# Performance work log

Measured on AMD Instinct MI355X. Metric: run time of the kernel, lower is better.

## Reference

```python
import jax, jax.numpy as jnp
import numpy as np

B, S, D_MODEL, D_FF = 4, 2048, 1024, 4096


def setup_inputs() -> dict:
    key = jax.random.key(0)
    ks = jax.random.split(key, 8)
    return {
        "x": jax.random.normal(ks[0], (B, S, D_MODEL), dtype=jnp.float32),
        "W1": jax.random.normal(ks[1], (D_MODEL, D_FF), dtype=jnp.float32) * (1.0 / np.sqrt(D_MODEL)),
        "b1": jnp.zeros((D_FF,), dtype=jnp.float32),
        "quantum_phases": jax.random.normal(ks[2], (D_FF,), dtype=jnp.float32) * (2.0 * np.pi),
        "quantum_weights_real": jax.random.normal(ks[3], (D_FF,), dtype=jnp.float32) * 0.1,
        "quantum_weights_imag": jax.random.normal(ks[4], (D_FF,), dtype=jnp.float32) * 0.1,
        "W2": jax.random.normal(ks[5], (D_FF, D_MODEL), dtype=jnp.float32) * (1.0 / np.sqrt(D_FF)),
        "b2": jnp.zeros((D_MODEL,), dtype=jnp.float32),
    }


def _quantum_transform(hidden, theta, w_real, w_imag):
    # hidden: [B,S,d_ff]; theta/w_real/w_imag: [d_ff] broadcast over channels
    imag = w_imag * jnp.sin(theta + hidden * 0.1)
    quantum_phase = jnp.cos(theta) * w_real + jnp.sin(theta) * w_imag  # [d_ff]
    return hidden + quantum_phase * imag * 0.1


def reference(x, W1, b1, quantum_phases, quantum_weights_real, quantum_weights_imag, W2, b2):
    hidden = jnp.einsum("bsd,df->bsf", x, W1) + b1  # [B,S,d_ff]
    q = _quantum_transform(hidden, quantum_phases, quantum_weights_real, quantum_weights_imag)
    act = jax.nn.relu(q)  # dropout is identity in eval mode
    return jnp.einsum("bsf,fd->bsd", act, W2) + b2
```

## Files before the change

### kernel.cpp

```cpp
#include <hip/hip_runtime.h>

typedef __bf16 bf16x8 __attribute__((ext_vector_type(8)));
typedef short  s16x8  __attribute__((ext_vector_type(8)));
typedef float  f32x4  __attribute__((ext_vector_type(4)));

#define DEVINL __device__ __forceinline__

DEVINL unsigned short f2bf(float f) {
  unsigned int u = __builtin_bit_cast(unsigned int, f);
  u += 0x7fffu + ((u >> 16) & 1u);
  return (unsigned short)(u >> 16);
}

DEVINL void async16(const void* g, void* l) {
  __builtin_amdgcn_global_load_lds(
      (const __attribute__((address_space(1))) unsigned int*)g,
      (__attribute__((address_space(3))) unsigned int*)l, 16, 0, 0);
}


__global__ void cvt_f32_bf16(const float* __restrict__ in,
                             unsigned short* __restrict__ out, int n4) {
  int i = blockIdx.x * blockDim.x + threadIdx.x;
  int stride = gridDim.x * blockDim.x;
  for (; i < n4; i += stride) {
    float4 v = ((const float4*)in)[i];
    ushort4 o;
    o.x = f2bf(v.x); o.y = f2bf(v.y); o.z = f2bf(v.z); o.w = f2bf(v.w);
    ((ushort4*)out)[i] = o;
  }
}

__global__ void transpose_cvt(const float* __restrict__ in,
                              unsigned short* __restrict__ out, int R, int C) {
  __shared__ unsigned short tile[32][33];
  int bc = blockIdx.x * 32, br = blockIdx.y * 32;
  int tx = threadIdx.x & 31, ty = threadIdx.x >> 5;
#pragma unroll
  for (int i = 0; i < 32; i += 8)
    tile[ty + i][tx] = f2bf(in[(size_t)(br + ty + i) * C + (bc + tx)]);
  __syncthreads();
#pragma unroll
  for (int i = 0; i < 32; i += 8)
    out[(size_t)(bc + ty + i) * R + (br + tx)] = tile[tx][ty + i];
}

__global__ void qconst(const float* __restrict__ theta,
                       const float* __restrict__ wre,
                       const float* __restrict__ wim,
                       float* __restrict__ c1, int n) {
  int i = blockIdx.x * blockDim.x + threadIdx.x;
  if (i < n) {
    float t = theta[i];
    c1[i] = (cosf(t) * wre[i] + sinf(t) * wim[i]) * wim[i] * 0.1f;
  }
}


template <int BM, int NT, bool FUSED>
__global__ __launch_bounds__(512, 2) void gemm8(
    const unsigned short* __restrict__ A,
    const unsigned short* __restrict__ Bt,
    const float* __restrict__ bias,
    const float* __restrict__ theta,
    const float* __restrict__ c1,
    void* __restrict__ Cout,
    int N, int nTilesN) {
  constexpr int K      = NT * 64;
  constexpr int WROWS  = BM / 2;
  constexpr int M_REP  = WROWS / 16;
  constexpr int MH     = M_REP / 2;
  constexpr int ABYTES = BM * 128;
  constexpr int AH     = ABYTES / 2;
  constexpr int AL     = AH / 8192;
  constexpr int BUFSZ  = ABYTES + 32768;
  static_assert(AL == 2 || AL == 1, "geometry");

  __shared__ __align__(16) char lds[2 * BUFSZ];

  int nwg = gridDim.x;
  int wg = blockIdx.x;
  int sw = (wg & 7) * (nwg >> 3) + (wg >> 3);
  int rowBase = (sw / nTilesN) * BM;
  int colBase = (sw % nTilesN) * 256;

  const int t = threadIdx.x;
  const int lane = t & 63;
  const int wid = t >> 6;
  const int wr = wid >> 2, wc = wid & 3;
  const int lr = lane & 15;
  const int lg = lane >> 4;
  const int r7 = lane & 7;

  const int srow = t >> 3;
  const int scolB = ((t & 7) * 16) ^ ((srow & 7) << 4);
  const unsigned short* aSrcB = A  + (size_t)(rowBase + srow) * K + (scolB >> 1);
  const unsigned short* bSrcB = Bt + (size_t)(colBase + srow) * K + (scolB >> 1);

  const int aRd = (wr * WROWS + lr) * 128 + ((lg ^ r7) << 4);
  const int bRd = ABYTES + (wc * 64 + lr) * 128 + ((lg ^ r7) << 4);

  f32x4 acc[M_REP][4] = {};
  bf16x8 a[MH][2], b[4][2];

#define STAGE_AU(S, U, P) do {                                              \
    _Pragma("unroll") for (int j = 0; j < AL; ++j)                          \
      async16(aSrcB + ((size_t)((U) * WROWS + j * 64) * K + (size_t)(S) * 64),\
              &lds[(P) * BUFSZ + (U) * AH + j * 8192 + t * 16]);            \
  } while (0)
#define STAGE_BU(S, U, P) do {                                              \
    _Pragma("unroll") for (int j = 0; j < 2; ++j)                           \
      async16(bSrcB + ((size_t)((U) * 128 + j * 64) * K + (size_t)(S) * 64),\
              &lds[(P) * BUFSZ + ABYTES + (U) * 16384 + j * 8192 + t * 16]);\
  } while (0)

#define LOAD_A(MHh, P)                                                      \
  _Pragma("unroll") for (int mi = 0; mi < MH; ++mi)                         \
  _Pragma("unroll") for (int ks = 0; ks < 2; ++ks)                          \
    a[mi][ks] = __builtin_bit_cast(bf16x8, *(const s16x8*)&lds[             \
        (P) * BUFSZ + ((aRd + ((MHh) * MH + mi) * 2048) ^ (ks << 6))])
#define LOAD_B(NHh, P)                                                      \
  _Pragma("unroll") for (int nn = 0; nn < 2; ++nn)                          \
  _Pragma("unroll") for (int ks = 0; ks < 2; ++ks)                          \
    b[(NHh) * 2 + nn][ks] = __builtin_bit_cast(bf16x8, *(const s16x8*)&lds[ \
        (P) * BUFSZ + ((bRd + ((NHh) * 2 + nn) * 2048) ^ (ks << 6))])

#define QUAD(MHh, NHh)                                                      \
  __builtin_amdgcn_s_setprio(1);                                            \
  _Pragma("unroll") for (int mi = 0; mi < MH; ++mi)                         \
  _Pragma("unroll") for (int nn = 0; nn < 2; ++nn)                          \
  _Pragma("unroll") for (int ks = 0; ks < 2; ++ks)                          \
    acc[(MHh) * MH + mi][(NHh) * 2 + nn] =                                  \
        __builtin_amdgcn_mfma_f32_16x16x32_bf16(                            \
            a[mi][ks], b[(NHh) * 2 + nn][ks],                               \
            acc[(MHh) * MH + mi][(NHh) * 2 + nn], 0, 0, 0);                 \
  __builtin_amdgcn_s_setprio(0)

#define BAR() __builtin_amdgcn_s_barrier()
#define LG0() asm volatile("s_waitcnt lgkmcnt(0)" ::: "memory")

#define TILE(T, P) do {                                                     \
                                                      \
    LOAD_A(0, P); LOAD_B(0, P);                                             \
    if ((T) + 1 < NT) STAGE_AU((T) + 1, 0, (P) ^ 1);                        \
    if (MH == 4) asm volatile("s_waitcnt lgkmcnt(8)" ::: "memory");         \
    BAR(); LG0(); QUAD(0, 0); BAR();                                        \
                                                      \
    LOAD_B(1, P);                                                           \
    if ((T) + 1 < NT) STAGE_AU((T) + 1, 1, (P) ^ 1);                        \
    BAR(); LG0(); QUAD(0, 1); BAR();                                        \
                                                      \
    LOAD_A(1, P);                                                           \
    if ((T) + 2 < NT) STAGE_BU((T) + 2, 0, P);                              \
    BAR(); LG0(); QUAD(1, 1); BAR();                                        \
                                    \
    if ((T) + 2 < NT) STAGE_BU((T) + 2, 1, P);                              \
    BAR(); QUAD(1, 0);                                                      \
    if ((T) + 2 < NT) {                                                     \
      asm volatile("s_waitcnt vmcnt(4)" ::: "memory");                      \
    } else if ((T) + 1 < NT) {                                              \
      asm volatile("s_waitcnt vmcnt(0)" ::: "memory");                      \
    }                                                                       \
    BAR();                                                                  \
  } while (0)

  STAGE_AU(0, 0, 0); STAGE_AU(0, 1, 0);
  STAGE_BU(0, 0, 0); STAGE_BU(0, 1, 0);
  STAGE_BU(1, 0, 1); STAGE_BU(1, 1, 1);
  asm volatile("s_waitcnt vmcnt(4)" ::: "memory");
  BAR();

  for (int T = 0; T < NT; T += 2) {
    TILE(T, 0);
    TILE(T + 1, 1);
  }

#undef TILE
#undef QUAD
#undef LOAD_A
#undef LOAD_B
#undef STAGE_AU
#undef STAGE_BU
#undef BAR
#undef LG0

  const int orow0 = rowBase + wr * WROWS + (lane >> 4) * 4;
  const int ocol0 = colBase + wc * 64 + lr;
#pragma unroll
  for (int ni = 0; ni < 4; ++ni) {
    int n = ocol0 + ni * 16;
    float bv = bias[n];
    float th = 0.f, cc = 0.f;
    if constexpr (FUSED) { th = theta[n]; cc = c1[n]; }
#pragma unroll
    for (int mi = 0; mi < M_REP; ++mi) {
#pragma unroll
      for (int r = 0; r < 4; ++r) {
        size_t m = (size_t)(orow0 + mi * 16 + r);
        float h = acc[mi][ni][r] + bv;
        if constexpr (FUSED) {
          float q = h + cc * __sinf(th + 0.1f * h);
          ((unsigned short*)Cout)[m * N + n] = f2bf(fmaxf(q, 0.f));
        } else {
          ((float*)Cout)[m * N + n] = h;
        }
      }
    }
  }
}


extern "C" void kernel_launch(void* const* d_in, const int* in_sizes, int n_in,
                              void* d_out, int out_size, void* d_ws,
                              size_t ws_size, hipStream_t stream) {
  const float* x     = (const float*)d_in[0];
  const float* W1    = (const float*)d_in[1];
  const float* b1    = (const float*)d_in[2];
  const float* theta = (const float*)d_in[3];
  const float* qwr   = (const float*)d_in[4];
  const float* qwi   = (const float*)d_in[5];
  const float* W2    = (const float*)d_in[6];
  const float* b2    = (const float*)d_in[7];
  float* out = (float*)d_out;

  const int M = 4 * 2048;
  const int DM = 1024, DF = 4096;

  size_t need = ((size_t)96 << 20) + DF * sizeof(float);
  if (ws_size < need) return;

  char* ws = (char*)d_ws;
  unsigned short* xb   = (unsigned short*)ws;
  unsigned short* w1t  = (unsigned short*)(ws + ((size_t)16 << 20));
  unsigned short* w2t  = (unsigned short*)(ws + ((size_t)24 << 20));
  unsigned short* actb = (unsigned short*)(ws + ((size_t)32 << 20));
  float* c1 = (float*)(ws + ((size_t)96 << 20));

  cvt_f32_bf16<<<2048, 256, 0, stream>>>(x, xb, M * DM / 4);
  transpose_cvt<<<dim3(DF / 32, DM / 32), 256, 0, stream>>>(W1, w1t, DM, DF);
  transpose_cvt<<<dim3(DM / 32, DF / 32), 256, 0, stream>>>(W2, w2t, DF, DM);
  qconst<<<DF / 256, 256, 0, stream>>>(theta, qwr, qwi, c1, DF);

  gemm8<256, 16, true><<<512, 512, 0, stream>>>(
      xb, w1t, b1, theta, c1, (void*)actb, DF, DF / 256);
  gemm8<128, 64, false><<<256, 512, 0, stream>>>(
      actb, w2t, b2, nullptr, nullptr, (void*)out, DM, DM / 256);
}
```

Baseline: 166.1 us.

## Make fused GEMM1 persistent over two column tiles and stage epilogue stores through LDS

GEMM1 now launches half as many workgroups, each handling two adjacent 256-column output tiles in sequence. The prologue loads for the second tile are issued before the first tile's epilogue, so the epilogue overlaps with the next loads. The fused epilogue writes bf16 results into an extra 16KB LDS scratch region with a swizzle, then emits 16-byte coalesced global stores instead of scattered 2-byte stores. The extra LDS may reduce occupancy, and the grid drops to 256 workgroups, which lowers parallelism.

```diff
diff --git a/kernel.cpp b/kernel.cpp
--- a/kernel.cpp
+++ b/kernel.cpp
@@ -57,7 +57,7 @@
 }
 
 
-template <int BM, int NT, bool FUSED>
+template <int BM, int NT, int REPS, bool FUSED>
 __global__ __launch_bounds__(512, 2) void gemm8(
     const unsigned short* __restrict__ A,
     const unsigned short* __restrict__ Bt,
@@ -74,15 +74,16 @@
   constexpr int AH     = ABYTES / 2;
   constexpr int AL     = AH / 8192;
   constexpr int BUFSZ  = ABYTES + 32768;
+  constexpr int LDSSZ  = 2 * BUFSZ + (FUSED ? 16384 : 0);
   static_assert(AL == 2 || AL == 1, "geometry");
 
-  __shared__ __align__(16) char lds[2 * BUFSZ];
+  __shared__ __align__(16) char lds[LDSSZ];
 
   int nwg = gridDim.x;
   int wg = blockIdx.x;
   int sw = (wg & 7) * (nwg >> 3) + (wg >> 3);
   int rowBase = (sw / nTilesN) * BM;
-  int colBase = (sw % nTilesN) * 256;
+  int colBase = (sw % nTilesN) * (256 * REPS);
 
   const int t = threadIdx.x;
   const int lane = t & 63;
@@ -100,17 +101,14 @@
   const int aRd = (wr * WROWS + lr) * 128 + ((lg ^ r7) << 4);
   const int bRd = ABYTES + (wc * 64 + lr) * 128 + ((lg ^ r7) << 4);
 
-  f32x4 acc[M_REP][4] = {};
-  bf16x8 a[MH][2], b[4][2];
-
 #define STAGE_AU(S, U, P) do {                                              \
     _Pragma("unroll") for (int j = 0; j < AL; ++j)                          \
       async16(aSrcB + ((size_t)((U) * WROWS + j * 64) * K + (size_t)(S) * 64),\
               &lds[(P) * BUFSZ + (U) * AH + j * 8192 + t * 16]);            \
   } while (0)
-#define STAGE_BU(S, U, P) do {                                              \
+#define STAGE_BU(SRC, S, U, P) do {                                         \
     _Pragma("unroll") for (int j = 0; j < 2; ++j)                           \
-      async16(bSrcB + ((size_t)((U) * 128 + j * 64) * K + (size_t)(S) * 64),\
+      async16((SRC) + ((size_t)((U) * 128 + j * 64) * K + (size_t)(S) * 64),\
               &lds[(P) * BUFSZ + ABYTES + (U) * 16384 + j * 8192 + t * 16]);\
   } while (0)
 
@@ -140,21 +138,17 @@
 #define LG0() asm volatile("s_waitcnt lgkmcnt(0)" ::: "memory")
 
 #define TILE(T, P) do {                                                     \
-                                                      \
     LOAD_A(0, P); LOAD_B(0, P);                                             \
     if ((T) + 1 < NT) STAGE_AU((T) + 1, 0, (P) ^ 1);                        \
     if (MH == 4) asm volatile("s_waitcnt lgkmcnt(8)" ::: "memory");         \
     BAR(); LG0(); QUAD(0, 0); BAR();                                        \
-                                                      \
     LOAD_B(1, P);                                                           \
     if ((T) + 1 < NT) STAGE_AU((T) + 1, 1, (P) ^ 1);                        \
     BAR(); LG0(); QUAD(0, 1); BAR();                                        \
-                                                      \
     LOAD_A(1, P);                                                           \
-    if ((T) + 2 < NT) STAGE_BU((T) + 2, 0, P);                              \
+    if ((T) + 2 < NT) STAGE_BU(bSrcR, (T) + 2, 0, P);                       \
     BAR(); LG0(); QUAD(1, 1); BAR();                                        \
-                                    \
-    if ((T) + 2 < NT) STAGE_BU((T) + 2, 1, P);                              \
+    if ((T) + 2 < NT) STAGE_BU(bSrcR, (T) + 2, 1, P);                       \
     BAR(); QUAD(1, 0);                                                      \
     if ((T) + 2 < NT) {                                                     \
       asm volatile("s_waitcnt vmcnt(4)" ::: "memory");                      \
@@ -165,14 +159,87 @@
   } while (0)
 
   STAGE_AU(0, 0, 0); STAGE_AU(0, 1, 0);
-  STAGE_BU(0, 0, 0); STAGE_BU(0, 1, 0);
-  STAGE_BU(1, 0, 1); STAGE_BU(1, 1, 1);
+  STAGE_BU(bSrcB, 0, 0, 0); STAGE_BU(bSrcB, 0, 1, 0);
+  STAGE_BU(bSrcB, 1, 0, 1); STAGE_BU(bSrcB, 1, 1, 1);
   asm volatile("s_waitcnt vmcnt(4)" ::: "memory");
   BAR();
 
-  for (int T = 0; T < NT; T += 2) {
-    TILE(T, 0);
-    TILE(T + 1, 1);
+  for (int rep = 0; rep < REPS; ++rep) {
+    const unsigned short* bSrcR = bSrcB + (size_t)rep * 256 * K;
+    f32x4 acc[M_REP][4] = {};
+    bf16x8 a[MH][2], b[4][2];
+
+    for (int T = 0; T < NT; T += 2) {
+      TILE(T, 0);
+      TILE(T + 1, 1);
+    }
+
+    if (rep + 1 < REPS) {
+      const unsigned short* bSrcN = bSrcB + (size_t)(rep + 1) * 256 * K;
+      STAGE_AU(0, 0, 0); STAGE_AU(0, 1, 0);
+      STAGE_BU(bSrcN, 0, 0, 0); STAGE_BU(bSrcN, 0, 1, 0);
+      STAGE_BU(bSrcN, 1, 0, 1); STAGE_BU(bSrcN, 1, 1, 1);
+    }
+
+    const int colR = colBase + rep * 256;
+    const int ocol0 = colR + wc * 64 + lr;
+    if constexpr (FUSED) {
+      float bvv[4], thv[4], ccv[4];
+#pragma unroll
+      for (int ni = 0; ni < 4; ++ni) {
+        int n = ocol0 + ni * 16;
+        bvv[ni] = bias[n]; thv[ni] = theta[n]; ccv[ni] = c1[n];
+      }
+      const int SB = 2 * BUFSZ + wid * 2048;
+      const int srw = lane >> 2;
+      const int sbyte = (lane & 3) * 32;
+      const size_t growB = (size_t)(rowBase + wr * WROWS) * N;
+      unsigned short* outp = (unsigned short*)Cout;
+#pragma unroll
+      for (int mi = 0; mi < M_REP; ++mi) {
+#pragma unroll
+        for (int ni = 0; ni < 4; ++ni) {
+#pragma unroll
+          for (int r = 0; r < 4; ++r) {
+            int row16 = lg * 4 + r;
+            float h = acc[mi][ni][r] + bvv[ni];
+            float q = h + ccv[ni] * __sinf(thv[ni] + 0.1f * h);
+            unsigned short v = f2bf(fmaxf(q, 0.f));
+            int ad = SB + row16 * 128 +
+                     (((ni * 16 + lr) * 2) ^ ((row16 & 7) << 4));
+            *(unsigned short*)&lds[ad] = v;
+          }
+        }
+        s16x8 w0 = *(const s16x8*)&lds[SB + srw * 128 +
+                                       ((sbyte) ^ ((srw & 7) << 4))];
+        s16x8 w1 = *(const s16x8*)&lds[SB + srw * 128 +
+                                       ((sbyte + 16) ^ ((srw & 7) << 4))];
+        unsigned short* dst = outp + growB + (size_t)(mi * 16 + srw) * N +
+                              colR + wc * 64 + (lane & 3) * 16;
+        *(s16x8*)dst = w0;
+        *(s16x8*)(dst + 8) = w1;
+      }
+    } else {
+      const int orow0 = rowBase + wr * WROWS + lg * 4;
+#pragma unroll
+      for (int ni = 0; ni < 4; ++ni) {
+        int n = ocol0 + ni * 16;
+        float bv = bias[n];
+#pragma unroll
+        for (int mi = 0; mi < M_REP; ++mi) {
+#pragma unroll
+          for (int r = 0; r < 4; ++r) {
+            size_t m = (size_t)(orow0 + mi * 16 + r);
+            ((float*)Cout)[m * N + n] = acc[mi][ni][r] + bv;
+          }
+        }
+      }
+    }
+
+    if (rep + 1 < REPS) {
+      asm volatile("s_waitcnt vmcnt(0)" ::: "memory");
+      BAR();
+    }
   }
 
 #undef TILE
@@ -183,30 +250,6 @@
 #undef STAGE_BU
 #undef BAR
 #undef LG0
-
-  const int orow0 = rowBase + wr * WROWS + (lane >> 4) * 4;
-  const int ocol0 = colBase + wc * 64 + lr;
-#pragma unroll
-  for (int ni = 0; ni < 4; ++ni) {
-    int n = ocol0 + ni * 16;
-    float bv = bias[n];
-    float th = 0.f, cc = 0.f;
-    if constexpr (FUSED) { th = theta[n]; cc = c1[n]; }
-#pragma unroll
-    for (int mi = 0; mi < M_REP; ++mi) {
-#pragma unroll
-      for (int r = 0; r < 4; ++r) {
-        size_t m = (size_t)(orow0 + mi * 16 + r);
-        float h = acc[mi][ni][r] + bv;
-        if constexpr (FUSED) {
-          float q = h + cc * __sinf(th + 0.1f * h);
-          ((unsigned short*)Cout)[m * N + n] = f2bf(fmaxf(q, 0.f));
-        } else {
-          ((float*)Cout)[m * N + n] = h;
-        }
-      }
-    }
-  }
 }
 
 
@@ -241,8 +284,8 @@
   transpose_cvt<<<dim3(DM / 32, DF / 32), 256, 0, stream>>>(W2, w2t, DF, DM);
   qconst<<<DF / 256, 256, 0, stream>>>(theta, qwr, qwi, c1, DF);
 
-  gemm8<256, 16, true><<<512, 512, 0, stream>>>(
-      xb, w1t, b1, theta, c1, (void*)actb, DF, DF / 256);
-  gemm8<128, 64, false><<<256, 512, 0, stream>>>(
+  gemm8<256, 16, 2, true><<<256, 512, 0, stream>>>(
+      xb, w1t, b1, theta, c1, (void*)actb, DF, DF / 512);
+  gemm8<128, 64, 1, false><<<256, 512, 0, stream>>>(
       actb, w2t, b2, nullptr, nullptr, (void*)out, DM, DM / 256);
 }
```

Result: no change. 168.7 us (+1.6%).
